# Optimization experiments

Measured on AMD Instinct MI355X. Metric: run time of the kernel, lower is better.

## Reference

```python
import jax, jax.numpy as jnp
import numpy as np


def setup_inputs() -> dict:
    key = jax.random.key(0)
    k1, k2 = jax.random.split(key)
    B, S, K, N = 8, 2048, 2048, 2048
    a = jax.random.normal(k1, (B, S, K), dtype=jnp.float32)
    b = jax.random.normal(k2, (B, K, N), dtype=jnp.float32)
    return {"a": a, "b": b}


def reference(a, b):
    # Per-sample dense: out[i] = a[i] @ b[i], fused as one batched GEMM.
    # a: [B, S, K], b: [B, K, N] -> out: [B, S, N]
    return jnp.einsum('bsk,bkn->bsn', a, b)
```

## Files before the change

kernel.cpp:

```cpp
#include <hip/hip_runtime.h>

#define BATCH 8
#define SDIM 2048
#define KDIM 2048
#define NDIM 2048

typedef __bf16 bf16_t;
typedef bf16_t bf16x4 __attribute__((ext_vector_type(4)));
typedef bf16_t bf16x8 __attribute__((ext_vector_type(8)));
typedef float f32x4 __attribute__((ext_vector_type(4)));
typedef float f32x8 __attribute__((ext_vector_type(8)));
typedef unsigned short u16x8 __attribute__((ext_vector_type(8)));

__device__ __forceinline__ void gl_lds16(const void* g, void* l) {
    __builtin_amdgcn_global_load_lds(
        (__attribute__((address_space(1))) void*)g,
        (__attribute__((address_space(3))) void*)l,
        16, 0, 0);
}

__global__ __launch_bounds__(256)
void cvtA_kernel(const float* __restrict__ A, bf16_t* __restrict__ Abf) {
    const size_t total8 = (size_t)BATCH * SDIM * KDIM / 8;
    const size_t stride = (size_t)gridDim.x * 256;
    for (size_t i = (size_t)blockIdx.x * 256 + threadIdx.x; i < total8; i += stride) {
        f32x8 v = *reinterpret_cast<const f32x8*>(A + i * 8);
        *reinterpret_cast<bf16x8*>(Abf + i * 8) = __builtin_convertvector(v, bf16x8);
    }
}

__global__ __launch_bounds__(256)
void cvtBT_kernel(const float* __restrict__ B, bf16_t* __restrict__ Bt) {
    __shared__ alignas(16) bf16_t T[64][72];
    const int gid = blockIdx.x;
    const int batch = gid & 7;
    const int tile = gid >> 3;
    const int k0g = (tile >> 5) * 64;
    const int n0g = (tile & 31) * 64;
    const float* Bb = B + (size_t)batch * KDIM * NDIM + (size_t)k0g * NDIM + n0g;
    bf16_t* Tb = Bt + (size_t)batch * NDIM * KDIM + (size_t)n0g * KDIM + k0g;

    const int t = threadIdx.x;
    const int kq = t & 15;
    const int nq = t >> 4;
    f32x4 v[4];
#pragma unroll
    for (int r = 0; r < 4; ++r)
        v[r] = *reinterpret_cast<const f32x4*>(Bb + (size_t)(kq * 4 + r) * NDIM + nq * 4);
#pragma unroll
    for (int j = 0; j < 4; ++j) {
        bf16x4 w = {(bf16_t)v[0][j], (bf16_t)v[1][j], (bf16_t)v[2][j], (bf16_t)v[3][j]};
        *reinterpret_cast<bf16x4*>(&T[nq * 4 + j][kq * 4]) = w;
    }
    __syncthreads();
    const int n = t >> 2, kc = t & 3;
    bf16x8 o0 = *reinterpret_cast<const bf16x8*>(&T[n][kc * 16]);
    bf16x8 o1 = *reinterpret_cast<const bf16x8*>(&T[n][kc * 16 + 8]);
    *reinterpret_cast<bf16x8*>(Tb + (size_t)n * KDIM + kc * 16) = o0;
    *reinterpret_cast<bf16x8*>(Tb + (size_t)n * KDIM + kc * 16 + 8) = o1;
}

#define VM8 asm volatile("s_waitcnt vmcnt(8)" ::: "memory")
#define VM4 asm volatile("s_waitcnt vmcnt(4)" ::: "memory")
#define VM0 asm volatile("s_waitcnt vmcnt(0)" ::: "memory")
#define NOOP ((void)0)

__global__ __launch_bounds__(512, 2)
void bgemm_ring(const bf16_t* __restrict__ A, const bf16_t* __restrict__ Bt,
                float* __restrict__ O) {
    __shared__ alignas(16) bf16_t lds[65536];

    const int tid = threadIdx.x;
    const int gid = blockIdx.x;
    const int batch = gid & 7;
    const int t = gid >> 3;
    const int bm = (t >> 3) * 256;
    const int bn = (t & 7) * 256;

    const int lane = tid & 63;
    const int wid = tid >> 6;
    const int wr = wid >> 2;
    const int wc = wid & 3;
    const int lr = lane & 15;
    const int lq = lane >> 4;

    const bf16_t* Ab = A + (size_t)batch * SDIM * KDIM;
    const bf16_t* Bb = Bt + (size_t)batch * NDIM * KDIM;
    float* Ob = O + (size_t)batch * SDIM * NDIM;

    const bf16_t* aSrc0 = Ab + (size_t)(bm + wid * 32 + lr) * KDIM + lq * 8;
    const bf16_t* aSrc1 = aSrc0 + (size_t)16 * KDIM;
    const bf16_t* bSrc0 = Bb + (size_t)(bn + wid * 32 + lr) * KDIM + lq * 8;
    const bf16_t* bSrc1 = bSrc0 + (size_t)16 * KDIM;

    const int aDst0 = (wid * 2) * 512;
    const int aDst1 = (wid * 2 + 1) * 512;
    const int rdA = lq * 128 + lr * 8;
    const int rdB = 8192 + lq * 128 + lr * 8;

#define STAGE(BUF_, KT_) do { \
    gl_lds16(aSrc0 + (size_t)(KT_) * 32, &lds[(BUF_) * 16384 + aDst0]); \
    gl_lds16(aSrc1 + (size_t)(KT_) * 32, &lds[(BUF_) * 16384 + aDst1]); \
    gl_lds16(bSrc0 + (size_t)(KT_) * 32, &lds[(BUF_) * 16384 + 8192 + aDst0]); \
    gl_lds16(bSrc1 + (size_t)(KT_) * 32, &lds[(BUF_) * 16384 + 8192 + aDst1]); \
} while (0)

    f32x4 acc[8][4];
#pragma unroll
    for (int m = 0; m < 8; ++m)
#pragma unroll
        for (int n = 0; n < 4; ++n)
            acc[m][n] = (f32x4){0.f, 0.f, 0.f, 0.f};

#define BODY(BUF_, STAGE_STMT, VM_STMT) do { \
    VM_STMT; \
    __builtin_amdgcn_s_barrier(); \
    STAGE_STMT; \
    bf16x8 af_[8], bf_[4]; \
    _Pragma("unroll") \
    for (int m_ = 0; m_ < 8; ++m_) \
        af_[m_] = *reinterpret_cast<const bf16x8*>( \
            &lds[(BUF_) * 16384 + (wr * 8 + m_) * 512 + rdA]); \
    _Pragma("unroll") \
    for (int n_ = 0; n_ < 4; ++n_) \
        bf_[n_] = *reinterpret_cast<const bf16x8*>( \
            &lds[(BUF_) * 16384 + (wc * 4 + n_) * 512 + rdB]); \
    __builtin_amdgcn_s_setprio(1); \
    _Pragma("unroll") \
    for (int m_ = 0; m_ < 8; ++m_) \
        _Pragma("unroll") \
        for (int n_ = 0; n_ < 4; ++n_) \
            acc[m_][n_] = __builtin_amdgcn_mfma_f32_16x16x32_bf16( \
                af_[m_], bf_[n_], acc[m_][n_], 0, 0, 0); \
    __builtin_amdgcn_s_setprio(0); \
} while (0)

    STAGE(0, 0);
    STAGE(1, 1);
    STAGE(2, 2);

#pragma unroll 1
    for (int j4 = 0; j4 < 60; j4 += 4) {
        BODY(0, STAGE(3, j4 + 3), VM8);
        BODY(1, STAGE(0, j4 + 4), VM8);
        BODY(2, STAGE(1, j4 + 5), VM8);
        BODY(3, STAGE(2, j4 + 6), VM8);
    }
    BODY(0, STAGE(3, 63), VM8);
    BODY(1, NOOP, VM8);
    BODY(2, NOOP, VM4);
    BODY(3, NOOP, VM0);

#pragma unroll
    for (int m = 0; m < 8; ++m) {
        const int row0 = bm + wr * 128 + m * 16 + lq * 4;
#pragma unroll
        for (int n = 0; n < 4; ++n) {
            const int col = bn + wc * 64 + n * 16 + lr;
#pragma unroll
            for (int j = 0; j < 4; ++j)
                Ob[(size_t)(row0 + j) * NDIM + col] = acc[m][n][j];
        }
    }
#undef BODY
#undef STAGE
}

__device__ __forceinline__ unsigned short f2bf(float f) {
    unsigned int u = __builtin_bit_cast(unsigned int, f);
    u += 0x7fffu + ((u >> 16) & 1u);
    return (unsigned short)(u >> 16);
}

__global__ __launch_bounds__(256, 2)
void bgemm_fused(const float* __restrict__ A, const float* __restrict__ B,
                 float* __restrict__ O) {
    __shared__ alignas(16) unsigned short Asl[2][4 * 128 * 8];
    __shared__ alignas(16) unsigned short Bsl[2][4 * 128 * 8];
    const int tid = threadIdx.x;
    const int gid = blockIdx.x;
    const int batch = gid & 7;
    const int t = gid >> 3;
    const int bm = (t >> 4) * 128;
    const int bn = (t & 15) * 128;
    const float* Ab = A + (size_t)batch * SDIM * KDIM;
    const float* Bb = B + (size_t)batch * KDIM * NDIM;
    float* Ob = O + (size_t)batch * SDIM * NDIM;
    const int lane = tid & 63;
    const int wid = tid >> 6;
    const int wr = wid >> 1, wc = wid & 1;
    const int lr = lane & 15, lq = lane >> 4;
    const int r0 = tid & 127, h0 = tid >> 7;
    u16x8 areg[2], breg[2];
    f32x4 acc[4][4];
#pragma unroll
    for (int m = 0; m < 4; ++m)
#pragma unroll
        for (int n = 0; n < 4; ++n) acc[m][n] = (f32x4){0.f, 0.f, 0.f, 0.f};
    auto stage_regs = [&](int kt) {
        const int k0 = kt * 32;
        const float* ap = Ab + (size_t)(bm + r0) * KDIM + k0 + h0 * 16;
        float4 a0 = *reinterpret_cast<const float4*>(ap + 0);
        float4 a1 = *reinterpret_cast<const float4*>(ap + 4);
        float4 a2 = *reinterpret_cast<const float4*>(ap + 8);
        float4 a3 = *reinterpret_cast<const float4*>(ap + 12);
        u16x8 u;
        u[0]=f2bf(a0.x);u[1]=f2bf(a0.y);u[2]=f2bf(a0.z);u[3]=f2bf(a0.w);
        u[4]=f2bf(a1.x);u[5]=f2bf(a1.y);u[6]=f2bf(a1.z);u[7]=f2bf(a1.w);
        areg[0]=u;
        u[0]=f2bf(a2.x);u[1]=f2bf(a2.y);u[2]=f2bf(a2.z);u[3]=f2bf(a2.w);
        u[4]=f2bf(a3.x);u[5]=f2bf(a3.y);u[6]=f2bf(a3.z);u[7]=f2bf(a3.w);
        areg[1]=u;
        const float* bp = Bb + (size_t)(k0 + h0 * 16) * NDIM + bn + r0;
        float f[16];
#pragma unroll
        for (int j = 0; j < 16; ++j) f[j] = bp[(size_t)j * NDIM];
        u16x8 v;
#pragma unroll
        for (int j = 0; j < 8; ++j) v[j] = f2bf(f[j]);
        breg[0] = v;
#pragma unroll
        for (int j = 0; j < 8; ++j) v[j] = f2bf(f[8 + j]);
        breg[1] = v;
    };
    auto regs_to_lds = [&](int b) {
#pragma unroll
        for (int o = 0; o < 2; ++o) {
            *reinterpret_cast<u16x8*>(&Asl[b][((h0*2+o)*128 + r0)*8]) = areg[o];
            *reinterpret_cast<u16x8*>(&Bsl[b][((h0*2+o)*128 + r0)*8]) = breg[o];
        }
    };
    stage_regs(0);
    regs_to_lds(0);
    int buf = 0;
    for (int kt = 0; kt < KDIM / 32; ++kt) {
        if (kt + 1 < KDIM / 32) stage_regs(kt + 1);
        __syncthreads();
        bf16x8 af[4], bfv[4];
#pragma unroll
        for (int m = 0; m < 4; ++m)
            af[m] = *reinterpret_cast<const bf16x8*>(&Asl[buf][(lq*128 + wr*64 + m*16 + lr)*8]);
#pragma unroll
        for (int n = 0; n < 4; ++n)
            bfv[n] = *reinterpret_cast<const bf16x8*>(&Bsl[buf][(lq*128 + wc*64 + n*16 + lr)*8]);
#pragma unroll
        for (int m = 0; m < 4; ++m)
#pragma unroll
            for (int n = 0; n < 4; ++n)
                acc[m][n] = __builtin_amdgcn_mfma_f32_16x16x32_bf16(af[m], bfv[n], acc[m][n], 0, 0, 0);
        if (kt + 1 < KDIM / 32) regs_to_lds(buf ^ 1);
        buf ^= 1;
    }
#pragma unroll
    for (int m = 0; m < 4; ++m) {
        const int row0 = bm + wr * 64 + m * 16 + lq * 4;
#pragma unroll
        for (int n = 0; n < 4; ++n) {
            const int col = bn + wc * 64 + n * 16 + lr;
#pragma unroll
            for (int j = 0; j < 4; ++j)
                Ob[(size_t)(row0 + j) * NDIM + col] = acc[m][n][j];
        }
    }
}

extern "C" void kernel_launch(void* const* d_in, const int* in_sizes, int n_in,
                              void* d_out, int out_size, void* d_ws, size_t ws_size,
                              hipStream_t stream) {
    const float* a = (const float*)d_in[0];
    const float* b = (const float*)d_in[1];
    float* o = (float*)d_out;
    const size_t half = (size_t)BATCH * SDIM * KDIM * sizeof(bf16_t);
    if (ws_size >= 2 * half) {
        bf16_t* Abf = (bf16_t*)d_ws;
        bf16_t* Bt = (bf16_t*)((char*)d_ws + half);
        hipLaunchKernelGGL(cvtA_kernel, dim3(4096), dim3(256), 0, stream, a, Abf);
        hipLaunchKernelGGL(cvtBT_kernel, dim3(8192), dim3(256), 0, stream, b, Bt);
        hipLaunchKernelGGL(bgemm_ring, dim3(512), dim3(512), 0, stream, Abf, Bt, o);
    } else {
        hipLaunchKernelGGL(bgemm_fused, dim3(2048), dim3(256), 0, stream, a, b, o);
    }
}
```

Measured before the change: 254.0 us.

## Split MFMA tile into halves and overlap LDS reads with MFMA across iterations

Restructures the GEMM main loop so each iteration first issues the upper-half MFMAs of the previous tile, then reads the next tile's lower A and B fragments, issues the global-to-LDS prefetch, reads the upper A fragments and runs the lower-half MFMAs. The intent is to hide LDS read latency behind matrix-core work. Prefetch depth drops from three tiles in flight to two, with the barrier moved to the end of each body. This reduces the latency slack for global loads and changes register pressure from holding fragments across iterations.

```diff
diff --git a/kernel.cpp b/kernel.cpp
--- a/kernel.cpp
+++ b/kernel.cpp
@@ -60,13 +60,12 @@
     *reinterpret_cast<bf16x8*>(Tb + (size_t)n * KDIM + kc * 16 + 8) = o1;
 }
 
-#define VM8 asm volatile("s_waitcnt vmcnt(8)" ::: "memory")
 #define VM4 asm volatile("s_waitcnt vmcnt(4)" ::: "memory")
 #define VM0 asm volatile("s_waitcnt vmcnt(0)" ::: "memory")
 #define NOOP ((void)0)
 
 __global__ __launch_bounds__(512, 2)
-void bgemm_ring(const bf16_t* __restrict__ A, const bf16_t* __restrict__ Bt,
+void bgemm_pipe(const bf16_t* __restrict__ A, const bf16_t* __restrict__ Bt,
                 float* __restrict__ O) {
     __shared__ alignas(16) bf16_t lds[65536];
 
@@ -112,44 +111,76 @@
         for (int n = 0; n < 4; ++n)
             acc[m][n] = (f32x4){0.f, 0.f, 0.f, 0.f};
 
-#define BODY(BUF_, STAGE_STMT, VM_STMT) do { \
-    VM_STMT; \
-    __builtin_amdgcn_s_barrier(); \
-    STAGE_STMT; \
-    bf16x8 af_[8], bf_[4]; \
-    _Pragma("unroll") \
-    for (int m_ = 0; m_ < 8; ++m_) \
-        af_[m_] = *reinterpret_cast<const bf16x8*>( \
+    bf16x8 aLo[4], aHi[4], bFr[4];
+
+#define READ_LOB(BUF_) do { \
+    _Pragma("unroll") \
+    for (int m_ = 0; m_ < 4; ++m_) \
+        aLo[m_] = *reinterpret_cast<const bf16x8*>( \
             &lds[(BUF_) * 16384 + (wr * 8 + m_) * 512 + rdA]); \
     _Pragma("unroll") \
     for (int n_ = 0; n_ < 4; ++n_) \
-        bf_[n_] = *reinterpret_cast<const bf16x8*>( \
+        bFr[n_] = *reinterpret_cast<const bf16x8*>( \
             &lds[(BUF_) * 16384 + (wc * 4 + n_) * 512 + rdB]); \
+} while (0)
+
+#define READ_HI(BUF_) do { \
+    _Pragma("unroll") \
+    for (int m_ = 0; m_ < 4; ++m_) \
+        aHi[m_] = *reinterpret_cast<const bf16x8*>( \
+            &lds[(BUF_) * 16384 + (wr * 8 + 4 + m_) * 512 + rdA]); \
+} while (0)
+
+#define MFMA_LO do { \
     __builtin_amdgcn_s_setprio(1); \
     _Pragma("unroll") \
-    for (int m_ = 0; m_ < 8; ++m_) \
+    for (int m_ = 0; m_ < 4; ++m_) \
         _Pragma("unroll") \
         for (int n_ = 0; n_ < 4; ++n_) \
             acc[m_][n_] = __builtin_amdgcn_mfma_f32_16x16x32_bf16( \
-                af_[m_], bf_[n_], acc[m_][n_], 0, 0, 0); \
+                aLo[m_], bFr[n_], acc[m_][n_], 0, 0, 0); \
     __builtin_amdgcn_s_setprio(0); \
+} while (0)
+
+#define MFMA_HI do { \
+    __builtin_amdgcn_s_setprio(1); \
+    _Pragma("unroll") \
+    for (int m_ = 0; m_ < 4; ++m_) \
+        _Pragma("unroll") \
+        for (int n_ = 0; n_ < 4; ++n_) \
+            acc[4 + m_][n_] = __builtin_amdgcn_mfma_f32_16x16x32_bf16( \
+                aHi[m_], bFr[n_], acc[4 + m_][n_], 0, 0, 0); \
+    __builtin_amdgcn_s_setprio(0); \
+} while (0)
+
+#define BODY(BUF_, J_, DO_HI_, DO_STAGE_, VM_STMT, DO_BAR_) do { \
+    if (DO_HI_) MFMA_HI; \
+    READ_LOB(BUF_); \
+    if (DO_STAGE_) STAGE(((J_) + 2) & 3, (J_) + 2); \
+    READ_HI(BUF_); \
+    MFMA_LO; \
+    VM_STMT; \
+    if (DO_BAR_) __builtin_amdgcn_s_barrier(); \
 } while (0)
 
     STAGE(0, 0);
     STAGE(1, 1);
-    STAGE(2, 2);
+    VM4;
+    __builtin_amdgcn_s_barrier();
+
+    BODY(0, 0, 0, 1, VM4, 1);
 
 #pragma unroll 1
-    for (int j4 = 0; j4 < 60; j4 += 4) {
-        BODY(0, STAGE(3, j4 + 3), VM8);
-        BODY(1, STAGE(0, j4 + 4), VM8);
-        BODY(2, STAGE(1, j4 + 5), VM8);
-        BODY(3, STAGE(2, j4 + 6), VM8);
-    }
-    BODY(0, STAGE(3, 63), VM8);
-    BODY(1, NOOP, VM8);
-    BODY(2, NOOP, VM4);
-    BODY(3, NOOP, VM0);
+    for (int j4 = 1; j4 < 61; j4 += 4) {
+        BODY(1, j4 + 0, 1, 1, VM4, 1);
+        BODY(2, j4 + 1, 1, 1, VM4, 1);
+        BODY(3, j4 + 2, 1, 1, VM4, 1);
+        BODY(0, j4 + 3, 1, 1, VM4, 1);
+    }
+    BODY(1, 61, 1, 1, VM4, 1);
+    BODY(2, 62, 1, 0, VM0, 1);
+    BODY(3, 63, 1, 0, NOOP, 0);
+    MFMA_HI;
 
 #pragma unroll
     for (int m = 0; m < 8; ++m) {
@@ -163,6 +194,10 @@
         }
     }
 #undef BODY
+#undef MFMA_HI
+#undef MFMA_LO
+#undef READ_HI
+#undef READ_LOB
 #undef STAGE
 }
 
@@ -276,7 +311,7 @@
         bf16_t* Bt = (bf16_t*)((char*)d_ws + half);
         hipLaunchKernelGGL(cvtA_kernel, dim3(4096), dim3(256), 0, stream, a, Abf);
         hipLaunchKernelGGL(cvtBT_kernel, dim3(8192), dim3(256), 0, stream, b, Bt);
-        hipLaunchKernelGGL(bgemm_ring, dim3(512), dim3(512), 0, stream, Abf, Bt, o);
+        hipLaunchKernelGGL(bgemm_pipe, dim3(512), dim3(512), 0, stream, Abf, Bt, o);
     } else {
         hipLaunchKernelGGL(bgemm_fused, dim3(2048), dim3(256), 0, stream, a, b, o);
     }
```

Measured after the change: 251.5 us. Within noise of the previous version (-1.0%).

## Restructure bf16 GEMM main loop into double-buffered K=64 tiles with quarter-phase scheduling

Applied to the files above, without the earlier changes.

The bf16 batched GEMM replaces its four-stage K=32 ring buffer with a two-buffer K=64 scheme. Each K step is split into four quadrant phases of LDS reads plus MFMAs, with global-to-LDS loads for the next tile interleaved between them. Barriers, sched_barriers and explicit lgkmcnt/vmcnt waits pin the instruction order so memory traffic overlaps matrix-core work. The extra barriers and the fixed schedule add synchronisation cost and could stall warps if the phases turn out unbalanced.

```diff
diff --git a/kernel.cpp b/kernel.cpp
--- a/kernel.cpp
+++ b/kernel.cpp
@@ -60,13 +60,15 @@
     *reinterpret_cast<bf16x8*>(Tb + (size_t)n * KDIM + kc * 16 + 8) = o1;
 }
 
-#define VM8 asm volatile("s_waitcnt vmcnt(8)" ::: "memory")
-#define VM4 asm volatile("s_waitcnt vmcnt(4)" ::: "memory")
+#define VM2 asm volatile("s_waitcnt vmcnt(2)" ::: "memory")
 #define VM0 asm volatile("s_waitcnt vmcnt(0)" ::: "memory")
+#define BAR __builtin_amdgcn_s_barrier()
+#define SB0 __builtin_amdgcn_sched_barrier(0)
+#define LG0 do { asm volatile("s_waitcnt lgkmcnt(0)" ::: "memory"); SB0; } while (0)
 #define NOOP ((void)0)
 
 __global__ __launch_bounds__(512, 2)
-void bgemm_ring(const bf16_t* __restrict__ A, const bf16_t* __restrict__ Bt,
+void bgemm_t201(const bf16_t* __restrict__ A, const bf16_t* __restrict__ Bt,
                 float* __restrict__ O) {
     __shared__ alignas(16) bf16_t lds[65536];
 
@@ -88,22 +90,15 @@
     const bf16_t* Bb = Bt + (size_t)batch * NDIM * KDIM;
     float* Ob = O + (size_t)batch * SDIM * NDIM;
 
-    const bf16_t* aSrc0 = Ab + (size_t)(bm + wid * 32 + lr) * KDIM + lq * 8;
-    const bf16_t* aSrc1 = aSrc0 + (size_t)16 * KDIM;
-    const bf16_t* bSrc0 = Bb + (size_t)(bn + wid * 32 + lr) * KDIM + lq * 8;
-    const bf16_t* bSrc1 = bSrc0 + (size_t)16 * KDIM;
-
-    const int aDst0 = (wid * 2) * 512;
-    const int aDst1 = (wid * 2 + 1) * 512;
-    const int rdA = lq * 128 + lr * 8;
-    const int rdB = 8192 + lq * 128 + lr * 8;
-
-#define STAGE(BUF_, KT_) do { \
-    gl_lds16(aSrc0 + (size_t)(KT_) * 32, &lds[(BUF_) * 16384 + aDst0]); \
-    gl_lds16(aSrc1 + (size_t)(KT_) * 32, &lds[(BUF_) * 16384 + aDst1]); \
-    gl_lds16(bSrc0 + (size_t)(KT_) * 32, &lds[(BUF_) * 16384 + 8192 + aDst0]); \
-    gl_lds16(bSrc1 + (size_t)(KT_) * 32, &lds[(BUF_) * 16384 + 8192 + aDst1]); \
-} while (0)
+    const bf16_t* aStg = Ab + (size_t)(bm + ((tid >> 7) << 4) + (tid & 15)) * KDIM
+                            + ((tid >> 4) & 7) * 8;
+    const bf16_t* bStg = Bb + (size_t)(bn + ((tid >> 7) << 4) + (tid & 15)) * KDIM
+                            + ((tid >> 4) & 7) * 8;
+
+#define STG_A(PD_, I_, KT_) gl_lds16(aStg + (size_t)(I_) * 64 * KDIM + (size_t)(KT_) * 64, \
+                                     &lds[(PD_) * 32768 + (I_) * 4096 + wid * 512])
+#define STG_B(PD_, I_, KT_) gl_lds16(bStg + (size_t)(I_) * 64 * KDIM + (size_t)(KT_) * 64, \
+                                     &lds[(PD_) * 32768 + 16384 + (I_) * 4096 + wid * 512])
 
     f32x4 acc[8][4];
 #pragma unroll
@@ -112,44 +107,77 @@
         for (int n = 0; n < 4; ++n)
             acc[m][n] = (f32x4){0.f, 0.f, 0.f, 0.f};
 
-#define BODY(BUF_, STAGE_STMT, VM_STMT) do { \
-    VM_STMT; \
-    __builtin_amdgcn_s_barrier(); \
-    STAGE_STMT; \
-    bf16x8 af_[8], bf_[4]; \
+    bf16x8 afr[4][2], b0f[2][2], b1f[2][2];
+
+#define RD_A(P_, MH_) do { \
     _Pragma("unroll") \
-    for (int m_ = 0; m_ < 8; ++m_) \
-        af_[m_] = *reinterpret_cast<const bf16x8*>( \
-            &lds[(BUF_) * 16384 + (wr * 8 + m_) * 512 + rdA]); \
+    for (int mq_ = 0; mq_ < 4; ++mq_) \
+        _Pragma("unroll") \
+        for (int ks_ = 0; ks_ < 2; ++ks_) \
+            afr[mq_][ks_] = *reinterpret_cast<const bf16x8*>( \
+                &lds[(P_) * 32768 + ((wr * 8 + (MH_) * 4 + mq_) * 128 \
+                                     + (ks_ * 4 + lq) * 16 + lr) * 8]); \
+} while (0)
+
+#define RD_B(P_, NH_, BF_) do { \
     _Pragma("unroll") \
-    for (int n_ = 0; n_ < 4; ++n_) \
-        bf_[n_] = *reinterpret_cast<const bf16x8*>( \
-            &lds[(BUF_) * 16384 + (wc * 4 + n_) * 512 + rdB]); \
+    for (int nq_ = 0; nq_ < 2; ++nq_) \
+        _Pragma("unroll") \
+        for (int ks_ = 0; ks_ < 2; ++ks_) \
+            BF_[nq_][ks_] = *reinterpret_cast<const bf16x8*>( \
+                &lds[(P_) * 32768 + 16384 + ((wc * 4 + (NH_) * 2 + nq_) * 128 \
+                                             + (ks_ * 4 + lq) * 16 + lr) * 8]); \
+} while (0)
+
+#define MFMA_Q(MB_, NB_, BF_) do { \
     __builtin_amdgcn_s_setprio(1); \
     _Pragma("unroll") \
-    for (int m_ = 0; m_ < 8; ++m_) \
+    for (int mq_ = 0; mq_ < 4; ++mq_) \
         _Pragma("unroll") \
-        for (int n_ = 0; n_ < 4; ++n_) \
-            acc[m_][n_] = __builtin_amdgcn_mfma_f32_16x16x32_bf16( \
-                af_[m_], bf_[n_], acc[m_][n_], 0, 0, 0); \
+        for (int nq_ = 0; nq_ < 2; ++nq_) \
+            _Pragma("unroll") \
+            for (int ks_ = 0; ks_ < 2; ++ks_) \
+                acc[(MB_) + mq_][(NB_) + nq_] = __builtin_amdgcn_mfma_f32_16x16x32_bf16( \
+                    afr[mq_][ks_], BF_[nq_][ks_], acc[(MB_) + mq_][(NB_) + nq_], 0, 0, 0); \
     __builtin_amdgcn_s_setprio(0); \
 } while (0)
 
-    STAGE(0, 0);
-    STAGE(1, 1);
-    STAGE(2, 2);
+#define BODY(P_, S1_, S2_, S3_, S0N_, VM_) do { \
+     SB0; RD_A(P_, 0); RD_B(P_, 0, b0f); S1_; SB0; BAR; LG0; \
+              MFMA_Q(0, 0, b0f); SB0; BAR; \
+     SB0; RD_B(P_, 1, b1f); S2_; SB0; BAR; LG0; \
+              MFMA_Q(0, 2, b1f); SB0; BAR; \
+     SB0; RD_A(P_, 1); S3_; SB0; BAR; LG0; \
+              MFMA_Q(4, 2, b1f); SB0; BAR; \
+     SB0; S0N_; VM_; SB0; BAR; SB0; \
+              MFMA_Q(4, 0, b0f); SB0; BAR; \
+} while (0)
+
+    STG_A(0, 0, 0); STG_A(0, 1, 0); STG_A(0, 2, 0); STG_A(0, 3, 0);
+    STG_B(0, 0, 0); STG_B(0, 1, 0); STG_B(0, 2, 0); STG_B(0, 3, 0);
+    STG_A(1, 0, 1); STG_A(1, 1, 1);
+    VM2;
+    BAR;
 
 #pragma unroll 1
-    for (int j4 = 0; j4 < 60; j4 += 4) {
-        BODY(0, STAGE(3, j4 + 3), VM8);
-        BODY(1, STAGE(0, j4 + 4), VM8);
-        BODY(2, STAGE(1, j4 + 5), VM8);
-        BODY(3, STAGE(2, j4 + 6), VM8);
-    }
-    BODY(0, STAGE(3, 63), VM8);
-    BODY(1, NOOP, VM8);
-    BODY(2, NOOP, VM4);
-    BODY(3, NOOP, VM0);
+    for (int j = 0; j < 30; j += 2) {
+        BODY(0,
+             (STG_A(1, 2, j + 1), STG_A(1, 3, j + 1)),
+             (STG_B(1, 0, j + 1), STG_B(1, 1, j + 1)),
+             (STG_B(1, 2, j + 1), STG_B(1, 3, j + 1)),
+             (STG_A(0, 0, j + 2), STG_A(0, 1, j + 2)), VM2);
+        BODY(1,
+             (STG_A(0, 2, j + 2), STG_A(0, 3, j + 2)),
+             (STG_B(0, 0, j + 2), STG_B(0, 1, j + 2)),
+             (STG_B(0, 2, j + 2), STG_B(0, 3, j + 2)),
+             (STG_A(1, 0, j + 3), STG_A(1, 1, j + 3)), VM2);
+    }
+    BODY(0,
+         (STG_A(1, 2, 31), STG_A(1, 3, 31)),
+         (STG_B(1, 0, 31), STG_B(1, 1, 31)),
+         (STG_B(1, 2, 31), STG_B(1, 3, 31)),
+         NOOP, VM0);
+    BODY(1, NOOP, NOOP, NOOP, NOOP, NOOP);
 
 #pragma unroll
     for (int m = 0; m < 8; ++m) {
@@ -163,7 +191,11 @@
         }
     }
 #undef BODY
-#undef STAGE
+#undef MFMA_Q
+#undef RD_B
+#undef RD_A
+#undef STG_B
+#undef STG_A
 }
 
 __device__ __forceinline__ unsigned short f2bf(float f) {
@@ -276,7 +308,7 @@
         bf16_t* Bt = (bf16_t*)((char*)d_ws + half);
         hipLaunchKernelGGL(cvtA_kernel, dim3(4096), dim3(256), 0, stream, a, Abf);
         hipLaunchKernelGGL(cvtBT_kernel, dim3(8192), dim3(256), 0, stream, b, Bt);
-        hipLaunchKernelGGL(bgemm_ring, dim3(512), dim3(512), 0, stream, Abf, Bt, o);
+        hipLaunchKernelGGL(bgemm_t201, dim3(512), dim3(512), 0, stream, Abf, Bt, o);
     } else {
         hipLaunchKernelGGL(bgemm_fused, dim3(2048), dim3(256), 0, stream, a, b, o);
     }
```

Measured after the change: 251.9 us. No clear change (-0.8%).

## Replace 4-stage ring GEMM with smaller-tile double-buffered kernel at higher occupancy

Applied to the files above, without the earlier changes.

The bf16 GEMM kernel moves from 256x256 tiles with a 4-deep LDS ring and 2 blocks per CU to 256x128 tiles with a 2-deep buffer and launch bounds for 4 blocks per CU, doubling the grid to 1024 blocks. Each wave now holds a 4x4 accumulator instead of 8x4, and each k-step adds a second barrier so the next stage can be prefetched into the buffer just read. The aim is to hide memory latency through more resident waves rather than deep software pipelining. In exchange, per-block operand reuse is lower, which raises global and LDS traffic per flop, and there are more barriers per k-step.

```diff
diff --git a/kernel.cpp b/kernel.cpp
--- a/kernel.cpp
+++ b/kernel.cpp
@@ -60,27 +60,28 @@
     *reinterpret_cast<bf16x8*>(Tb + (size_t)n * KDIM + kc * 16 + 8) = o1;
 }
 
-#define VM8 asm volatile("s_waitcnt vmcnt(8)" ::: "memory")
-#define VM4 asm volatile("s_waitcnt vmcnt(4)" ::: "memory")
+#define VM3 asm volatile("s_waitcnt vmcnt(3)" ::: "memory")
 #define VM0 asm volatile("s_waitcnt vmcnt(0)" ::: "memory")
-#define NOOP ((void)0)
-
-__global__ __launch_bounds__(512, 2)
-void bgemm_ring(const bf16_t* __restrict__ A, const bf16_t* __restrict__ Bt,
-                float* __restrict__ O) {
-    __shared__ alignas(16) bf16_t lds[65536];
+#define LG0 asm volatile("s_waitcnt lgkmcnt(0)" ::: "memory")
+#define BAR __builtin_amdgcn_s_barrier()
+#define SB0 __builtin_amdgcn_sched_barrier(0)
+
+__global__ __launch_bounds__(512, 4)
+void bgemm_tlp(const bf16_t* __restrict__ A, const bf16_t* __restrict__ Bt,
+               float* __restrict__ O) {
+    __shared__ alignas(16) bf16_t lds[24576];
 
     const int tid = threadIdx.x;
     const int gid = blockIdx.x;
     const int batch = gid & 7;
     const int t = gid >> 3;
-    const int bm = (t >> 3) * 256;
-    const int bn = (t & 7) * 256;
+    const int bm = (t >> 4) * 256;
+    const int bn = (t & 15) * 128;
 
     const int lane = tid & 63;
     const int wid = tid >> 6;
-    const int wr = wid >> 2;
-    const int wc = wid & 3;
+    const int wr = wid >> 1;
+    const int wc = wid & 1;
     const int lr = lane & 15;
     const int lq = lane >> 4;
 
@@ -88,72 +89,66 @@
     const bf16_t* Bb = Bt + (size_t)batch * NDIM * KDIM;
     float* Ob = O + (size_t)batch * SDIM * NDIM;
 
-    const bf16_t* aSrc0 = Ab + (size_t)(bm + wid * 32 + lr) * KDIM + lq * 8;
-    const bf16_t* aSrc1 = aSrc0 + (size_t)16 * KDIM;
-    const bf16_t* bSrc0 = Bb + (size_t)(bn + wid * 32 + lr) * KDIM + lq * 8;
-    const bf16_t* bSrc1 = bSrc0 + (size_t)16 * KDIM;
-
-    const int aDst0 = (wid * 2) * 512;
-    const int aDst1 = (wid * 2 + 1) * 512;
-    const int rdA = lq * 128 + lr * 8;
-    const int rdB = 8192 + lq * 128 + lr * 8;
+    const bf16_t* aStg = Ab + (size_t)(bm + wid * 16 + lr) * KDIM + lq * 8;
+    const bf16_t* bStg = Bb + (size_t)(bn + wid * 16 + lr) * KDIM + lq * 8;
 
 #define STAGE(BUF_, KT_) do { \
-    gl_lds16(aSrc0 + (size_t)(KT_) * 32, &lds[(BUF_) * 16384 + aDst0]); \
-    gl_lds16(aSrc1 + (size_t)(KT_) * 32, &lds[(BUF_) * 16384 + aDst1]); \
-    gl_lds16(bSrc0 + (size_t)(KT_) * 32, &lds[(BUF_) * 16384 + 8192 + aDst0]); \
-    gl_lds16(bSrc1 + (size_t)(KT_) * 32, &lds[(BUF_) * 16384 + 8192 + aDst1]); \
+    gl_lds16(aStg + (size_t)(KT_) * 32,                      &lds[(BUF_) * 12288 + wid * 512]); \
+    gl_lds16(aStg + 128 * (size_t)KDIM + (size_t)(KT_) * 32, &lds[(BUF_) * 12288 + 4096 + wid * 512]); \
+    gl_lds16(bStg + (size_t)(KT_) * 32,                      &lds[(BUF_) * 12288 + 8192 + wid * 512]); \
 } while (0)
 
-    f32x4 acc[8][4];
-#pragma unroll
-    for (int m = 0; m < 8; ++m)
+    f32x4 acc[4][4];
+#pragma unroll
+    for (int m = 0; m < 4; ++m)
 #pragma unroll
         for (int n = 0; n < 4; ++n)
             acc[m][n] = (f32x4){0.f, 0.f, 0.f, 0.f};
 
-#define BODY(BUF_, STAGE_STMT, VM_STMT) do { \
-    VM_STMT; \
-    __builtin_amdgcn_s_barrier(); \
-    STAGE_STMT; \
-    bf16x8 af_[8], bf_[4]; \
+    const int rdA = lane * 8;
+    const int rdB = 8192 + lane * 8;
+
+#define TILE(P_, J_, DOSTAGE_, VM_) do { \
+    VM_; \
+    BAR; \
+    SB0; \
+    bf16x8 af_[4], bf_[4]; \
     _Pragma("unroll") \
-    for (int m_ = 0; m_ < 8; ++m_) \
-        af_[m_] = *reinterpret_cast<const bf16x8*>( \
-            &lds[(BUF_) * 16384 + (wr * 8 + m_) * 512 + rdA]); \
+    for (int mf_ = 0; mf_ < 4; ++mf_) \
+        af_[mf_] = *reinterpret_cast<const bf16x8*>( \
+            &lds[(P_) * 12288 + (wr * 4 + mf_) * 512 + rdA]); \
     _Pragma("unroll") \
-    for (int n_ = 0; n_ < 4; ++n_) \
-        bf_[n_] = *reinterpret_cast<const bf16x8*>( \
-            &lds[(BUF_) * 16384 + (wc * 4 + n_) * 512 + rdB]); \
+    for (int nf_ = 0; nf_ < 4; ++nf_) \
+        bf_[nf_] = *reinterpret_cast<const bf16x8*>( \
+            &lds[(P_) * 12288 + (wc * 4 + nf_) * 512 + rdB]); \
+    LG0; \
+    SB0; \
+    BAR; \
+    if (DOSTAGE_) STAGE(P_, (J_) + 2); \
     __builtin_amdgcn_s_setprio(1); \
     _Pragma("unroll") \
-    for (int m_ = 0; m_ < 8; ++m_) \
+    for (int mf_ = 0; mf_ < 4; ++mf_) \
         _Pragma("unroll") \
-        for (int n_ = 0; n_ < 4; ++n_) \
-            acc[m_][n_] = __builtin_amdgcn_mfma_f32_16x16x32_bf16( \
-                af_[m_], bf_[n_], acc[m_][n_], 0, 0, 0); \
+        for (int nf_ = 0; nf_ < 4; ++nf_) \
+            acc[mf_][nf_] = __builtin_amdgcn_mfma_f32_16x16x32_bf16( \
+                af_[mf_], bf_[nf_], acc[mf_][nf_], 0, 0, 0); \
     __builtin_amdgcn_s_setprio(0); \
 } while (0)
 
     STAGE(0, 0);
     STAGE(1, 1);
-    STAGE(2, 2);
 
 #pragma unroll 1
-    for (int j4 = 0; j4 < 60; j4 += 4) {
-        BODY(0, STAGE(3, j4 + 3), VM8);
-        BODY(1, STAGE(0, j4 + 4), VM8);
-        BODY(2, STAGE(1, j4 + 5), VM8);
-        BODY(3, STAGE(2, j4 + 6), VM8);
-    }
-    BODY(0, STAGE(3, 63), VM8);
-    BODY(1, NOOP, VM8);
-    BODY(2, NOOP, VM4);
-    BODY(3, NOOP, VM0);
-
-#pragma unroll
-    for (int m = 0; m < 8; ++m) {
-        const int row0 = bm + wr * 128 + m * 16 + lq * 4;
+    for (int j = 0; j < 62; j += 2) {
+        TILE(0, j, 1, VM3);
+        TILE(1, j + 1, 1, VM3);
+    }
+    TILE(0, 62, 0, VM3);
+    TILE(1, 63, 0, VM0);
+
+#pragma unroll
+    for (int m = 0; m < 4; ++m) {
+        const int row0 = bm + wr * 64 + m * 16 + lq * 4;
 #pragma unroll
         for (int n = 0; n < 4; ++n) {
             const int col = bn + wc * 64 + n * 16 + lr;
@@ -162,7 +157,7 @@
                 Ob[(size_t)(row0 + j) * NDIM + col] = acc[m][n][j];
         }
     }
-#undef BODY
+#undef TILE
 #undef STAGE
 }
 
@@ -276,7 +271,7 @@
         bf16_t* Bt = (bf16_t*)((char*)d_ws + half);
         hipLaunchKernelGGL(cvtA_kernel, dim3(4096), dim3(256), 0, stream, a, Abf);
         hipLaunchKernelGGL(cvtBT_kernel, dim3(8192), dim3(256), 0, stream, b, Bt);
-        hipLaunchKernelGGL(bgemm_ring, dim3(512), dim3(512), 0, stream, Abf, Bt, o);
+        hipLaunchKernelGGL(bgemm_tlp, dim3(1024), dim3(512), 0, stream, Abf, Bt, o);
     } else {
         hipLaunchKernelGGL(bgemm_fused, dim3(2048), dim3(256), 0, stream, a, b, o);
     }
```

Result: slower. 302.0 us (+18.9%).
